# Kernel tuning notes

Measured on AMD Instinct MI355X. Metric: run time of the kernel, lower is better.

Reference implementation:

```python
import jax, jax.numpy as jnp
import numpy as np

C = 64
NUM_GROUPS = 16  # per Normalize() logic for in_channels=64
EPS = 1e-5

def group_norm(x, gamma, beta):
    b, c, h, w, d = x.shape
    xg = x.reshape(b, NUM_GROUPS, c // NUM_GROUPS, h, w, d)
    mean = xg.mean(axis=(2, 3, 4, 5), keepdims=True)
    var = xg.var(axis=(2, 3, 4, 5), keepdims=True)
    xg = (xg - mean) * jax.lax.rsqrt(var + EPS)
    xn = xg.reshape(b, c, h, w, d)
    return xn * gamma[None, :, None, None, None] + beta[None, :, None, None, None]

def conv1x1(x, w, b):
    # 1x1x1 conv3d == channel mixing: w is [out_c, in_c]
    return jnp.einsum('bchwd,oc->bohwd', x, w) + b[None, :, None, None, None]

def setup_inputs() -> dict:
    key = jax.random.key(0)
    ks = jax.random.split(key, 11)
    s = 1.0 / np.sqrt(C)
    return {
        'x': jax.random.normal(ks[0], (2, C, 16, 16, 16), dtype=jnp.float32),
        'norm_w': jnp.ones((C,), jnp.float32),
        'norm_b': jnp.zeros((C,), jnp.float32),
        'q_w': jax.random.uniform(ks[1], (C, C), jnp.float32, -s, s),
        'q_b': jax.random.uniform(ks[2], (C,), jnp.float32, -s, s),
        'k_w': jax.random.uniform(ks[3], (C, C), jnp.float32, -s, s),
        'k_b': jax.random.uniform(ks[4], (C,), jnp.float32, -s, s),
        'v_w': jax.random.uniform(ks[5], (C, C), jnp.float32, -s, s),
        'v_b': jax.random.uniform(ks[6], (C,), jnp.float32, -s, s),
        'proj_w': jax.random.uniform(ks[7], (C, C), jnp.float32, -s, s),
        'proj_b': jax.random.uniform(ks[8], (C,), jnp.float32, -s, s),
    }

def reference(x, norm_w, norm_b, q_w, q_b, k_w, k_b, v_w, v_b, proj_w, proj_b):
    b, c, h, w, d = x.shape
    n = h * w * d
    hn = group_norm(x, norm_w, norm_b)
    q = conv1x1(hn, q_w, q_b).reshape(b, c, n)   # [b, c, n]
    k = conv1x1(hn, k_w, k_b).reshape(b, c, n)
    v = conv1x1(hn, v_w, v_b).reshape(b, c, n)
    scale = c ** (-0.5)
    scores = jnp.einsum('bcq,bck->bqk', q, k) * scale   # [b, n_q, n_k]
    attn = jax.nn.softmax(scores, axis=2)
    out = jnp.einsum('bck,bqk->bcq', v, attn)            # [b, c, n]
    out = out.reshape(b, c, h, w, d)
    out = conv1x1(out, proj_w, proj_b)
    return x + out
```

## Files before the change

kernel.cpp:

```cpp
#include <hip/hip_runtime.h>
#include <hip/hip_bf16.h>

#define B 2
#define C 64
#define N 4096
#define EPS 1e-5f
#define QSCALE_LOG2E 0.18033688f

using short8 = __attribute__((ext_vector_type(8))) short;
using f32x16 = __attribute__((ext_vector_type(16))) float;

__device__ inline short f2bf(float f) {
  __hip_bfloat16 h = __float2bfloat16(f);
  union { __hip_bfloat16 h; short s; } u; u.h = h; return u.s;
}
__device__ inline float bf2f(short s) {
  union { unsigned u; float f; } u;
  u.u = ((unsigned)(unsigned short)s) << 16;
  return u.f;
}
__device__ inline int packbf(float a, float b) {
  return (int)((unsigned short)f2bf(a) | ((unsigned)(unsigned short)f2bf(b) << 16));
}

__global__ __launch_bounds__(256) void gn_part_kernel(
    const float* __restrict__ x, float2* __restrict__ part) {
  int blk = blockIdx.x;
  int bg = blk >> 4, sl = blk & 15;
  const float4* xv = (const float4*)(x + (size_t)bg * 4 * N) + sl * 256;
  int tid = threadIdx.x;
  float4 v = xv[tid];
  float s = v.x + v.y + v.z + v.w;
  float s2 = v.x * v.x + v.y * v.y + v.z * v.z + v.w * v.w;
  __shared__ float ss[256], ss2[256];
  ss[tid] = s; ss2[tid] = s2;
  __syncthreads();
  for (int st = 128; st > 0; st >>= 1) {
    if (tid < st) { ss[tid] += ss[tid + st]; ss2[tid] += ss2[tid + st]; }
    __syncthreads();
  }
  if (tid == 0) part[blk] = make_float2(ss[0], ss2[0]);
}

__global__ __launch_bounds__(128) void gn_final_kernel(
    const float2* __restrict__ part, const float* __restrict__ gw,
    const float* __restrict__ gb, float* __restrict__ ascale,
    float* __restrict__ bshift) {
  int t = threadIdx.x;
  int c = t & 63, b = t >> 6, g = c >> 2;
  int bg = b * 16 + g;
  float s = 0.f, s2 = 0.f;
#pragma unroll
  for (int sl = 0; sl < 16; ++sl) {
    float2 p = part[bg * 16 + sl];
    s += p.x; s2 += p.y;
  }
  float mean = s * (1.f / 16384.f);
  float var = s2 * (1.f / 16384.f) - mean * mean;
  float inv = rsqrtf(var + EPS);
  float a = inv * gw[c];
  ascale[t] = a;
  bshift[t] = gb[c] - mean * a;
}

__global__ __launch_bounds__(256) void qkv_kernel(
    const float* __restrict__ x, const float* __restrict__ ascale,
    const float* __restrict__ bshift,
    const float* __restrict__ qw, const float* __restrict__ qb,
    const float* __restrict__ kw, const float* __restrict__ kb,
    const float* __restrict__ vw, const float* __restrict__ vb,
    short* __restrict__ q_t, short* __restrict__ k_t, short* __restrict__ v_b) {
  int o0 = blockIdx.y * 8, b = blockIdx.z;
  int pos = blockIdx.x * 256 + threadIdx.x;
  const float* xp = x + (size_t)b * C * N + pos;
  const float* as = ascale + b * C;
  const float* bs = bshift + b * C;

  float sq[8], sk[8], sv[8];
#pragma unroll
  for (int j = 0; j < 8; ++j) { sq[j] = 0.f; sk[j] = 0.f; sv[j] = 0.f; }
#pragma unroll
  for (int c = 0; c < C; ++c) {
    float hv = fmaf(xp[(size_t)c * N], as[c], bs[c]);
#pragma unroll
    for (int j = 0; j < 8; ++j) {
      sq[j] = fmaf(qw[(o0 + j) * C + c], hv, sq[j]);
      sk[j] = fmaf(kw[(o0 + j) * C + c], hv, sk[j]);
      sv[j] = fmaf(vw[(o0 + j) * C + c], hv, sv[j]);
    }
  }
  size_t ti = ((size_t)b * N + pos) * C;
  short8 qv, kv;
#pragma unroll
  for (int j = 0; j < 8; ++j) {
    qv[j] = f2bf((sq[j] + qb[o0 + j]) * QSCALE_LOG2E);
    kv[j] = f2bf(sk[j] + kb[o0 + j]);
  }
  *(short8*)&q_t[ti + o0] = qv;
  *(short8*)&k_t[ti + o0] = kv;
#pragma unroll
  for (int j = 0; j < 8; ++j)
    v_b[((size_t)b * C + o0 + j) * N + pos] = f2bf(sv[j] + vb[o0 + j]);
}

__device__ inline void softpack(f32x16& s, int hi, float& lsum,
                                short8& p0, short8& p1) {
  float ps = 0.f;
#pragma unroll
  for (int i = 0; i < 16; ++i) { s[i] = exp2f(s[i]); ps += s[i]; }
  lsum += ps;
  union U { int i[4]; short8 v; } f0, f1;
  {
    int x0 = packbf(s[0], s[1]), z0 = packbf(s[2], s[3]);
    int y0 = packbf(s[4], s[5]), w0 = packbf(s[6], s[7]);
    int xs = __shfl_xor(x0, 32), zs = __shfl_xor(z0, 32);
    int ys = __shfl_xor(y0, 32), ws2 = __shfl_xor(w0, 32);
    f0.i[0] = hi ? ys : x0; f0.i[1] = hi ? ws2 : z0;
    f0.i[2] = hi ? y0 : xs; f0.i[3] = hi ? w0 : zs;
  }
  {
    int x0 = packbf(s[8], s[9]), z0 = packbf(s[10], s[11]);
    int y0 = packbf(s[12], s[13]), w0 = packbf(s[14], s[15]);
    int xs = __shfl_xor(x0, 32), zs = __shfl_xor(z0, 32);
    int ys = __shfl_xor(y0, 32), ws2 = __shfl_xor(w0, 32);
    f1.i[0] = hi ? ys : x0; f1.i[1] = hi ? ws2 : z0;
    f1.i[2] = hi ? y0 : xs; f1.i[3] = hi ? w0 : zs;
  }
  p0 = f0.v; p1 = f1.v;
}

__global__ __launch_bounds__(256) void attn_kernel(
    const short* __restrict__ q_t, const short* __restrict__ k_t,
    const short* __restrict__ v_b, short* __restrict__ opart,
    float* __restrict__ lpart, int segLen, int kseg) {
  int b = blockIdx.z, s = blockIdx.y;
  int l = threadIdx.x & 63;
  int q0 = blockIdx.x * 256 + (threadIdx.x >> 6) * 64;
  int lo5 = l & 31;
  int hi = l >> 5;

  const short* qp = q_t + (size_t)b * N * C;
  const short* kp = k_t + (size_t)b * N * C;
  const short* vp = v_b + (size_t)b * C * N;

  short8 qf[2][4];
#pragma unroll
  for (int qt = 0; qt < 2; ++qt)
#pragma unroll
    for (int t = 0; t < 4; ++t)
      qf[qt][t] = *(const short8*)&qp[(size_t)(q0 + qt * 32 + lo5) * C + t * 16 + hi * 8];

  f32x16 oacc00, oacc01, oacc10, oacc11;
#pragma unroll
  for (int i = 0; i < 16; ++i) { oacc00[i] = 0.f; oacc01[i] = 0.f; oacc10[i] = 0.f; oacc11[i] = 0.f; }
  float lsum[2] = {0.f, 0.f};

  int kbase = s * segLen;

#define LOAD_KF(DST, K0)                                                     \
  _Pragma("unroll") for (int t = 0; t < 4; ++t)                              \
      DST[t] = *(const short8*)&kp[(size_t)((K0) + lo5) * C + t * 16 + hi * 8];
#define LOAD_VF(DST, K0)                                                     \
  DST[0] = *(const short8*)&vp[(size_t)(lo5) * N + (K0) + hi * 8];           \
  DST[1] = *(const short8*)&vp[(size_t)(32 + lo5) * N + (K0) + hi * 8];      \
  DST[2] = *(const short8*)&vp[(size_t)(lo5) * N + (K0) + 16 + hi * 8];      \
  DST[3] = *(const short8*)&vp[(size_t)(32 + lo5) * N + (K0) + 16 + hi * 8];

#define CHUNK(KF, VF)                                                        \
  {                                                                          \
    f32x16 s0_, s1_;                                                         \
    _Pragma("unroll") for (int i = 0; i < 16; ++i) { s0_[i] = 0.f; s1_[i] = 0.f; } \
    __builtin_amdgcn_s_setprio(1);                                           \
    _Pragma("unroll") for (int t = 0; t < 4; ++t) {                          \
      s0_ = __builtin_amdgcn_mfma_f32_32x32x16_bf16(KF[t], qf[0][t], s0_, 0, 0, 0); \
      s1_ = __builtin_amdgcn_mfma_f32_32x32x16_bf16(KF[t], qf[1][t], s1_, 0, 0, 0); \
    }                                                                        \
    __builtin_amdgcn_s_setprio(0);                                           \
    short8 pf00, pf01, pf10, pf11;                                           \
    softpack(s0_, hi, lsum[0], pf00, pf01);                                  \
    softpack(s1_, hi, lsum[1], pf10, pf11);                                  \
    __builtin_amdgcn_s_setprio(1);                                           \
    oacc00 = __builtin_amdgcn_mfma_f32_32x32x16_bf16(VF[0], pf00, oacc00, 0, 0, 0); \
    oacc01 = __builtin_amdgcn_mfma_f32_32x32x16_bf16(VF[1], pf00, oacc01, 0, 0, 0); \
    oacc10 = __builtin_amdgcn_mfma_f32_32x32x16_bf16(VF[0], pf10, oacc10, 0, 0, 0); \
    oacc11 = __builtin_amdgcn_mfma_f32_32x32x16_bf16(VF[1], pf10, oacc11, 0, 0, 0); \
    oacc00 = __builtin_amdgcn_mfma_f32_32x32x16_bf16(VF[2], pf01, oacc00, 0, 0, 0); \
    oacc01 = __builtin_amdgcn_mfma_f32_32x32x16_bf16(VF[3], pf01, oacc01, 0, 0, 0); \
    oacc10 = __builtin_amdgcn_mfma_f32_32x32x16_bf16(VF[2], pf11, oacc10, 0, 0, 0); \
    oacc11 = __builtin_amdgcn_mfma_f32_32x32x16_bf16(VF[3], pf11, oacc11, 0, 0, 0); \
    __builtin_amdgcn_s_setprio(0);                                           \
  }

  short8 kf0[4], kf1[4], vf0[4], vf1[4];
  LOAD_KF(kf0, kbase)
  LOAD_VF(vf0, kbase)

  for (int kc = 0; kc < segLen; kc += 64) {
    int kA = kbase + kc;
    LOAD_KF(kf1, kA + 32)
    LOAD_VF(vf1, kA + 32)
    CHUNK(kf0, vf0)
    int kN = (kc + 64 < segLen) ? (kA + 64) : kA;
    LOAD_KF(kf0, kN)
    LOAD_VF(vf0, kN)
    CHUNK(kf1, vf1)
  }

#pragma unroll
  for (int qt = 0; qt < 2; ++qt) {
    lsum[qt] += __shfl_xor(lsum[qt], 32);
    int qq = q0 + qt * 32 + lo5;
    short* op = opart + (size_t)(b * kseg + s) * C * N;
#pragma unroll
    for (int r = 0; r < 16; ++r) {
      int c = (r & 3) + 8 * (r >> 2) + 4 * hi;
      float v0 = (qt == 0) ? oacc00[r] : oacc10[r];
      float v1 = (qt == 0) ? oacc01[r] : oacc11[r];
      op[(size_t)c * N + qq] = f2bf(v0);
      op[(size_t)(c + 32) * N + qq] = f2bf(v1);
    }
    if (hi == 0) lpart[(size_t)(b * kseg + s) * N + qq] = lsum[qt];
  }
#undef LOAD_KF
#undef LOAD_VF
#undef CHUNK
}

__global__ __launch_bounds__(256) void merge_kernel(
    const short* __restrict__ opart, const float* __restrict__ lpart,
    short* __restrict__ attnout, int kseg) {
  int idx = blockIdx.x * 256 + threadIdx.x;
  int q4 = (idx & 1023) * 4;
  int c = (idx >> 10) & 63;
  int b = idx >> 16;

  float o[4] = {0.f, 0.f, 0.f, 0.f};
  float L[4] = {0.f, 0.f, 0.f, 0.f};
  for (int s = 0; s < kseg; ++s) {
    float4 lv = *(const float4*)&lpart[(size_t)(b * kseg + s) * N + q4];
    L[0] += lv.x; L[1] += lv.y; L[2] += lv.z; L[3] += lv.w;
    short4 ov = *(const short4*)&opart[((size_t)(b * kseg + s) * C + c) * N + q4];
    o[0] += bf2f(ov.x); o[1] += bf2f(ov.y); o[2] += bf2f(ov.z); o[3] += bf2f(ov.w);
  }
  short4 r;
  r.x = f2bf(o[0] / L[0]); r.y = f2bf(o[1] / L[1]);
  r.z = f2bf(o[2] / L[2]); r.w = f2bf(o[3] / L[3]);
  *(short4*)&attnout[(size_t)(b * C + c) * N + q4] = r;
}

__global__ __launch_bounds__(256) void proj_kernel(
    const short* __restrict__ at, const float* __restrict__ pw,
    const float* __restrict__ pb, const float* __restrict__ x,
    float* __restrict__ out) {
  int o0 = blockIdx.y * 8, b = blockIdx.z;
  int pos = blockIdx.x * 256 + threadIdx.x;
  const short* h = at + (size_t)b * C * N + pos;
  float sum[8];
#pragma unroll
  for (int j = 0; j < 8; ++j) sum[j] = 0.f;
#pragma unroll
  for (int c = 0; c < C; ++c) {
    float hv = bf2f(h[(size_t)c * N]);
#pragma unroll
    for (int j = 0; j < 8; ++j) sum[j] = fmaf(pw[(o0 + j) * C + c], hv, sum[j]);
  }
#pragma unroll
  for (int j = 0; j < 8; ++j) {
    size_t oi = (size_t)(b * C + o0 + j) * N + pos;
    out[oi] = x[oi] + sum[j] + pb[o0 + j];
  }
}

extern "C" void kernel_launch(void* const* d_in, const int* in_sizes, int n_in,
                              void* d_out, int out_size, void* d_ws, size_t ws_size,
                              hipStream_t stream) {
  const float* x      = (const float*)d_in[0];
  const float* norm_w = (const float*)d_in[1];
  const float* norm_b = (const float*)d_in[2];
  const float* q_w    = (const float*)d_in[3];
  const float* q_b    = (const float*)d_in[4];
  const float* k_w    = (const float*)d_in[5];
  const float* k_b    = (const float*)d_in[6];
  const float* v_w    = (const float*)d_in[7];
  const float* v_b    = (const float*)d_in[8];
  const float* proj_w = (const float*)d_in[9];
  const float* proj_b = (const float*)d_in[10];
  float* out = (float*)d_out;

  const size_t BCN = (size_t)B * C * N;

  int kseg = 16;
  auto need = [&](int s) -> size_t {
    return BCN * 2 * 4
         + (2 * B * C + 1024 + (size_t)s * B * N) * 4
         + (size_t)s * BCN * 2;
  };
  while (kseg > 1 && need(kseg) > ws_size) kseg >>= 1;
  int segLen = N / kseg;

  short* q_t     = (short*)d_ws;
  short* k_t     = q_t + BCN;
  short* vbuf    = k_t + BCN;
  short* attnout = vbuf + BCN;
  float* ascale  = (float*)(attnout + BCN);
  float* bshift  = ascale + B * C;
  float2* part   = (float2*)(bshift + B * C);
  float* lpart   = (float*)(part + 512);
  short* opart   = (short*)(lpart + (size_t)kseg * B * N);

  gn_part_kernel<<<512, 256, 0, stream>>>(x, part);
  gn_final_kernel<<<1, 128, 0, stream>>>(part, norm_w, norm_b, ascale, bshift);

  qkv_kernel<<<dim3(N / 256, C / 8, B), 256, 0, stream>>>(
      x, ascale, bshift, q_w, q_b, k_w, k_b, v_w, v_b, q_t, k_t, vbuf);

  attn_kernel<<<dim3(N / 256, kseg, B), 256, 0, stream>>>(
      q_t, k_t, vbuf, opart, lpart, segLen, kseg);

  merge_kernel<<<(int)(BCN / 4 / 256), 256, 0, stream>>>(
      opart, lpart, attnout, kseg);

  proj_kernel<<<dim3(N / 256, C / 8, B), 256, 0, stream>>>(
      attnout, proj_w, proj_b, x, out);
}
```

Measured before the change: 77.09 us.

## Fuse GN finalize into QKV, merge into projection, and simplify attention loop

New measurement: 92.95 us. 1.21x slower.

```diff
diff --git a/kernel.cpp b/kernel.cpp
--- a/kernel.cpp
+++ b/kernel.cpp
@@ -5,6 +5,8 @@
 #define C 64
 #define N 4096
 #define EPS 1e-5f
+#define KSEG 16
+#define SEGLEN 256
 #define QSCALE_LOG2E 0.18033688f
 
 using short8 = __attribute__((ext_vector_type(8))) short;
@@ -19,8 +21,10 @@
   u.u = ((unsigned)(unsigned short)s) << 16;
   return u.f;
 }
-__device__ inline int packbf(float a, float b) {
-  return (int)((unsigned short)f2bf(a) | ((unsigned)(unsigned short)f2bf(b) << 16));
+__device__ inline int cvtpk(float a, float b) {
+  int r;
+  asm("v_cvt_pk_bf16_f32 %0, %1, %2" : "=v"(r) : "v"(a), "v"(b));
+  return r;
 }
 
 __global__ __launch_bounds__(256) void gn_part_kernel(
@@ -42,46 +46,44 @@
   if (tid == 0) part[blk] = make_float2(ss[0], ss2[0]);
 }
 
-__global__ __launch_bounds__(128) void gn_final_kernel(
-    const float2* __restrict__ part, const float* __restrict__ gw,
-    const float* __restrict__ gb, float* __restrict__ ascale,
-    float* __restrict__ bshift) {
-  int t = threadIdx.x;
-  int c = t & 63, b = t >> 6, g = c >> 2;
-  int bg = b * 16 + g;
-  float s = 0.f, s2 = 0.f;
-#pragma unroll
-  for (int sl = 0; sl < 16; ++sl) {
-    float2 p = part[bg * 16 + sl];
-    s += p.x; s2 += p.y;
-  }
-  float mean = s * (1.f / 16384.f);
-  float var = s2 * (1.f / 16384.f) - mean * mean;
-  float inv = rsqrtf(var + EPS);
-  float a = inv * gw[c];
-  ascale[t] = a;
-  bshift[t] = gb[c] - mean * a;
-}
-
 __global__ __launch_bounds__(256) void qkv_kernel(
-    const float* __restrict__ x, const float* __restrict__ ascale,
-    const float* __restrict__ bshift,
+    const float* __restrict__ x, const float2* __restrict__ part,
+    const float* __restrict__ gw, const float* __restrict__ gb,
     const float* __restrict__ qw, const float* __restrict__ qb,
     const float* __restrict__ kw, const float* __restrict__ kb,
     const float* __restrict__ vw, const float* __restrict__ vb,
     short* __restrict__ q_t, short* __restrict__ k_t, short* __restrict__ v_b) {
   int o0 = blockIdx.y * 8, b = blockIdx.z;
-  int pos = blockIdx.x * 256 + threadIdx.x;
+  int tid = threadIdx.x;
+
+  __shared__ float asl[C], bsl[C];
+  if (tid < C) {
+    int c = tid, g = c >> 2;
+    int bg = b * 16 + g;
+    float s = 0.f, s2 = 0.f;
+#pragma unroll
+    for (int sl = 0; sl < 16; ++sl) {
+      float2 p = part[bg * 16 + sl];
+      s += p.x; s2 += p.y;
+    }
+    float mean = s * (1.f / 16384.f);
+    float var = s2 * (1.f / 16384.f) - mean * mean;
+    float inv = rsqrtf(var + EPS);
+    float a = inv * gw[c];
+    asl[c] = a;
+    bsl[c] = gb[c] - mean * a;
+  }
+  __syncthreads();
+
+  int pos = blockIdx.x * 256 + tid;
   const float* xp = x + (size_t)b * C * N + pos;
-  const float* as = ascale + b * C;
-  const float* bs = bshift + b * C;
 
   float sq[8], sk[8], sv[8];
 #pragma unroll
   for (int j = 0; j < 8; ++j) { sq[j] = 0.f; sk[j] = 0.f; sv[j] = 0.f; }
 #pragma unroll
   for (int c = 0; c < C; ++c) {
-    float hv = fmaf(xp[(size_t)c * N], as[c], bs[c]);
+    float hv = fmaf(xp[(size_t)c * N], asl[c], bsl[c]);
 #pragma unroll
     for (int j = 0; j < 8; ++j) {
       sq[j] = fmaf(qw[(o0 + j) * C + c], hv, sq[j]);
@@ -111,16 +113,16 @@
   lsum += ps;
   union U { int i[4]; short8 v; } f0, f1;
   {
-    int x0 = packbf(s[0], s[1]), z0 = packbf(s[2], s[3]);
-    int y0 = packbf(s[4], s[5]), w0 = packbf(s[6], s[7]);
+    int x0 = cvtpk(s[0], s[1]), z0 = cvtpk(s[2], s[3]);
+    int y0 = cvtpk(s[4], s[5]), w0 = cvtpk(s[6], s[7]);
     int xs = __shfl_xor(x0, 32), zs = __shfl_xor(z0, 32);
     int ys = __shfl_xor(y0, 32), ws2 = __shfl_xor(w0, 32);
     f0.i[0] = hi ? ys : x0; f0.i[1] = hi ? ws2 : z0;
     f0.i[2] = hi ? y0 : xs; f0.i[3] = hi ? w0 : zs;
   }
   {
-    int x0 = packbf(s[8], s[9]), z0 = packbf(s[10], s[11]);
-    int y0 = packbf(s[12], s[13]), w0 = packbf(s[14], s[15]);
+    int x0 = cvtpk(s[8], s[9]), z0 = cvtpk(s[10], s[11]);
+    int y0 = cvtpk(s[12], s[13]), w0 = cvtpk(s[14], s[15]);
     int xs = __shfl_xor(x0, 32), zs = __shfl_xor(z0, 32);
     int ys = __shfl_xor(y0, 32), ws2 = __shfl_xor(w0, 32);
     f1.i[0] = hi ? ys : x0; f1.i[1] = hi ? ws2 : z0;
@@ -129,10 +131,10 @@
   p0 = f0.v; p1 = f1.v;
 }
 
-__global__ __launch_bounds__(256) void attn_kernel(
+__global__ __launch_bounds__(256, 2) void attn_kernel(
     const short* __restrict__ q_t, const short* __restrict__ k_t,
     const short* __restrict__ v_b, short* __restrict__ opart,
-    float* __restrict__ lpart, int segLen, int kseg) {
+    float* __restrict__ lpart) {
   int b = blockIdx.z, s = blockIdx.y;
   int l = threadIdx.x & 63;
   int q0 = blockIdx.x * 256 + (threadIdx.x >> 6) * 64;
@@ -155,62 +157,51 @@
   for (int i = 0; i < 16; ++i) { oacc00[i] = 0.f; oacc01[i] = 0.f; oacc10[i] = 0.f; oacc11[i] = 0.f; }
   float lsum[2] = {0.f, 0.f};
 
-  int kbase = s * segLen;
-
-#define LOAD_KF(DST, K0)                                                     \
-  _Pragma("unroll") for (int t = 0; t < 4; ++t)                              \
-      DST[t] = *(const short8*)&kp[(size_t)((K0) + lo5) * C + t * 16 + hi * 8];
-#define LOAD_VF(DST, K0)                                                     \
-  DST[0] = *(const short8*)&vp[(size_t)(lo5) * N + (K0) + hi * 8];           \
-  DST[1] = *(const short8*)&vp[(size_t)(32 + lo5) * N + (K0) + hi * 8];      \
-  DST[2] = *(const short8*)&vp[(size_t)(lo5) * N + (K0) + 16 + hi * 8];      \
-  DST[3] = *(const short8*)&vp[(size_t)(32 + lo5) * N + (K0) + 16 + hi * 8];
-
-#define CHUNK(KF, VF)                                                        \
-  {                                                                          \
-    f32x16 s0_, s1_;                                                         \
-    _Pragma("unroll") for (int i = 0; i < 16; ++i) { s0_[i] = 0.f; s1_[i] = 0.f; } \
-    __builtin_amdgcn_s_setprio(1);                                           \
-    _Pragma("unroll") for (int t = 0; t < 4; ++t) {                          \
-      s0_ = __builtin_amdgcn_mfma_f32_32x32x16_bf16(KF[t], qf[0][t], s0_, 0, 0, 0); \
-      s1_ = __builtin_amdgcn_mfma_f32_32x32x16_bf16(KF[t], qf[1][t], s1_, 0, 0, 0); \
-    }                                                                        \
-    __builtin_amdgcn_s_setprio(0);                                           \
-    short8 pf00, pf01, pf10, pf11;                                           \
-    softpack(s0_, hi, lsum[0], pf00, pf01);                                  \
-    softpack(s1_, hi, lsum[1], pf10, pf11);                                  \
-    __builtin_amdgcn_s_setprio(1);                                           \
-    oacc00 = __builtin_amdgcn_mfma_f32_32x32x16_bf16(VF[0], pf00, oacc00, 0, 0, 0); \
-    oacc01 = __builtin_amdgcn_mfma_f32_32x32x16_bf16(VF[1], pf00, oacc01, 0, 0, 0); \
-    oacc10 = __builtin_amdgcn_mfma_f32_32x32x16_bf16(VF[0], pf10, oacc10, 0, 0, 0); \
-    oacc11 = __builtin_amdgcn_mfma_f32_32x32x16_bf16(VF[1], pf10, oacc11, 0, 0, 0); \
-    oacc00 = __builtin_amdgcn_mfma_f32_32x32x16_bf16(VF[2], pf01, oacc00, 0, 0, 0); \
-    oacc01 = __builtin_amdgcn_mfma_f32_32x32x16_bf16(VF[3], pf01, oacc01, 0, 0, 0); \
-    oacc10 = __builtin_amdgcn_mfma_f32_32x32x16_bf16(VF[2], pf11, oacc10, 0, 0, 0); \
-    oacc11 = __builtin_amdgcn_mfma_f32_32x32x16_bf16(VF[3], pf11, oacc11, 0, 0, 0); \
-    __builtin_amdgcn_s_setprio(0);                                           \
-  }
-
-  short8 kf0[4], kf1[4], vf0[4], vf1[4];
-  LOAD_KF(kf0, kbase)
-  LOAD_VF(vf0, kbase)
-
-  for (int kc = 0; kc < segLen; kc += 64) {
-    int kA = kbase + kc;
-    LOAD_KF(kf1, kA + 32)
-    LOAD_VF(vf1, kA + 32)
-    CHUNK(kf0, vf0)
-    int kN = (kc + 64 < segLen) ? (kA + 64) : kA;
-    LOAD_KF(kf0, kN)
-    LOAD_VF(vf0, kN)
-    CHUNK(kf1, vf1)
+  int kbase = s * SEGLEN;
+  for (int kc = 0; kc < SEGLEN; kc += 32) {
+    int k0 = kbase + kc;
+    short8 kf[4];
+#pragma unroll
+    for (int t = 0; t < 4; ++t)
+      kf[t] = *(const short8*)&kp[(size_t)(k0 + lo5) * C + t * 16 + hi * 8];
+    short8 vf[4];
+    vf[0] = *(const short8*)&vp[(size_t)(lo5) * N + k0 + hi * 8];
+    vf[1] = *(const short8*)&vp[(size_t)(32 + lo5) * N + k0 + hi * 8];
+    vf[2] = *(const short8*)&vp[(size_t)(lo5) * N + k0 + 16 + hi * 8];
+    vf[3] = *(const short8*)&vp[(size_t)(32 + lo5) * N + k0 + 16 + hi * 8];
+
+    f32x16 sacc[2];
+#pragma unroll
+    for (int i = 0; i < 16; ++i) { sacc[0][i] = 0.f; sacc[1][i] = 0.f; }
+    __builtin_amdgcn_s_setprio(1);
+#pragma unroll
+    for (int t = 0; t < 4; ++t) {
+      sacc[0] = __builtin_amdgcn_mfma_f32_32x32x16_bf16(kf[t], qf[0][t], sacc[0], 0, 0, 0);
+      sacc[1] = __builtin_amdgcn_mfma_f32_32x32x16_bf16(kf[t], qf[1][t], sacc[1], 0, 0, 0);
+    }
+    __builtin_amdgcn_s_setprio(0);
+
+    short8 pf00, pf01, pf10, pf11;
+    softpack(sacc[0], hi, lsum[0], pf00, pf01);
+    softpack(sacc[1], hi, lsum[1], pf10, pf11);
+
+    __builtin_amdgcn_s_setprio(1);
+    oacc00 = __builtin_amdgcn_mfma_f32_32x32x16_bf16(vf[0], pf00, oacc00, 0, 0, 0);
+    oacc01 = __builtin_amdgcn_mfma_f32_32x32x16_bf16(vf[1], pf00, oacc01, 0, 0, 0);
+    oacc10 = __builtin_amdgcn_mfma_f32_32x32x16_bf16(vf[0], pf10, oacc10, 0, 0, 0);
+    oacc11 = __builtin_amdgcn_mfma_f32_32x32x16_bf16(vf[1], pf10, oacc11, 0, 0, 0);
+    oacc00 = __builtin_amdgcn_mfma_f32_32x32x16_bf16(vf[2], pf01, oacc00, 0, 0, 0);
+    oacc01 = __builtin_amdgcn_mfma_f32_32x32x16_bf16(vf[3], pf01, oacc01, 0, 0, 0);
+    oacc10 = __builtin_amdgcn_mfma_f32_32x32x16_bf16(vf[2], pf11, oacc10, 0, 0, 0);
+    oacc11 = __builtin_amdgcn_mfma_f32_32x32x16_bf16(vf[3], pf11, oacc11, 0, 0, 0);
+    __builtin_amdgcn_s_setprio(0);
   }
 
 #pragma unroll
   for (int qt = 0; qt < 2; ++qt) {
     lsum[qt] += __shfl_xor(lsum[qt], 32);
     int qq = q0 + qt * 32 + lo5;
-    short* op = opart + (size_t)(b * kseg + s) * C * N;
+    short* op = opart + (size_t)(b * KSEG + s) * C * N;
 #pragma unroll
     for (int r = 0; r < 16; ++r) {
       int c = (r & 3) + 8 * (r >> 2) + 4 * hi;
@@ -219,55 +210,43 @@
       op[(size_t)c * N + qq] = f2bf(v0);
       op[(size_t)(c + 32) * N + qq] = f2bf(v1);
     }
-    if (hi == 0) lpart[(size_t)(b * kseg + s) * N + qq] = lsum[qt];
-  }
-#undef LOAD_KF
-#undef LOAD_VF
-#undef CHUNK
-}
-
-__global__ __launch_bounds__(256) void merge_kernel(
+    if (hi == 0) lpart[(size_t)(b * KSEG + s) * N + qq] = lsum[qt];
+  }
+}
+
+__global__ __launch_bounds__(256) void mergeproj_kernel(
     const short* __restrict__ opart, const float* __restrict__ lpart,
-    short* __restrict__ attnout, int kseg) {
-  int idx = blockIdx.x * 256 + threadIdx.x;
-  int q4 = (idx & 1023) * 4;
-  int c = (idx >> 10) & 63;
-  int b = idx >> 16;
-
-  float o[4] = {0.f, 0.f, 0.f, 0.f};
-  float L[4] = {0.f, 0.f, 0.f, 0.f};
-  for (int s = 0; s < kseg; ++s) {
-    float4 lv = *(const float4*)&lpart[(size_t)(b * kseg + s) * N + q4];
-    L[0] += lv.x; L[1] += lv.y; L[2] += lv.z; L[3] += lv.w;
-    short4 ov = *(const short4*)&opart[((size_t)(b * kseg + s) * C + c) * N + q4];
-    o[0] += bf2f(ov.x); o[1] += bf2f(ov.y); o[2] += bf2f(ov.z); o[3] += bf2f(ov.w);
-  }
-  short4 r;
-  r.x = f2bf(o[0] / L[0]); r.y = f2bf(o[1] / L[1]);
-  r.z = f2bf(o[2] / L[2]); r.w = f2bf(o[3] / L[3]);
-  *(short4*)&attnout[(size_t)(b * C + c) * N + q4] = r;
-}
-
-__global__ __launch_bounds__(256) void proj_kernel(
-    const short* __restrict__ at, const float* __restrict__ pw,
-    const float* __restrict__ pb, const float* __restrict__ x,
-    float* __restrict__ out) {
-  int o0 = blockIdx.y * 8, b = blockIdx.z;
-  int pos = blockIdx.x * 256 + threadIdx.x;
-  const short* h = at + (size_t)b * C * N + pos;
-  float sum[8];
-#pragma unroll
-  for (int j = 0; j < 8; ++j) sum[j] = 0.f;
+    const float* __restrict__ pw, const float* __restrict__ pb,
+    const float* __restrict__ x, float* __restrict__ out) {
+  int b = blockIdx.z;
+  int pos = blockIdx.x * 64 + (threadIdx.x & 63);
+  int o0 = blockIdx.y * 32 + (threadIdx.x >> 6) * 8;
+
+  float L = 0.f;
+#pragma unroll
+  for (int s = 0; s < KSEG; ++s) L += lpart[(size_t)(b * KSEG + s) * N + pos];
+  float invL = 1.f / L;
+
+  float acc[8];
+#pragma unroll
+  for (int j = 0; j < 8; ++j) acc[j] = 0.f;
+
+  const short* opb = opart + (size_t)b * KSEG * C * N + pos;
 #pragma unroll
   for (int c = 0; c < C; ++c) {
-    float hv = bf2f(h[(size_t)c * N]);
-#pragma unroll
-    for (int j = 0; j < 8; ++j) sum[j] = fmaf(pw[(o0 + j) * C + c], hv, sum[j]);
+    float a = 0.f;
+#pragma unroll
+    for (int s = 0; s < KSEG; ++s)
+      a += bf2f(opb[((size_t)s * C + c) * N]);
+    a *= invL;
+#pragma unroll
+    for (int j = 0; j < 8; ++j)
+      acc[j] = fmaf(pw[(o0 + j) * C + c], a, acc[j]);
   }
 #pragma unroll
   for (int j = 0; j < 8; ++j) {
     size_t oi = (size_t)(b * C + o0 + j) * N + pos;
-    out[oi] = x[oi] + sum[j] + pb[o0 + j];
+    out[oi] = x[oi] + acc[j] + pb[o0 + j];
   }
 }
 
@@ -288,38 +267,21 @@
   float* out = (float*)d_out;
 
   const size_t BCN = (size_t)B * C * N;
-
-  int kseg = 16;
-  auto need = [&](int s) -> size_t {
-    return BCN * 2 * 4
-         + (2 * B * C + 1024 + (size_t)s * B * N) * 4
-         + (size_t)s * BCN * 2;
-  };
-  while (kseg > 1 && need(kseg) > ws_size) kseg >>= 1;
-  int segLen = N / kseg;
-
-  short* q_t     = (short*)d_ws;
-  short* k_t     = q_t + BCN;
-  short* vbuf    = k_t + BCN;
-  short* attnout = vbuf + BCN;
-  float* ascale  = (float*)(attnout + BCN);
-  float* bshift  = ascale + B * C;
-  float2* part   = (float2*)(bshift + B * C);
-  float* lpart   = (float*)(part + 512);
-  short* opart   = (short*)(lpart + (size_t)kseg * B * N);
+  short* q_t   = (short*)d_ws;
+  short* k_t   = q_t + BCN;
+  short* vbuf  = k_t + BCN;
+  float2* part = (float2*)(vbuf + BCN);
+  float* lpart = (float*)(part + 512);
+  short* opart = (short*)(lpart + (size_t)KSEG * B * N);
 
   gn_part_kernel<<<512, 256, 0, stream>>>(x, part);
-  gn_final_kernel<<<1, 128, 0, stream>>>(part, norm_w, norm_b, ascale, bshift);
 
   qkv_kernel<<<dim3(N / 256, C / 8, B), 256, 0, stream>>>(
-      x, ascale, bshift, q_w, q_b, k_w, k_b, v_w, v_b, q_t, k_t, vbuf);
-
-  attn_kernel<<<dim3(N / 256, kseg, B), 256, 0, stream>>>(
-      q_t, k_t, vbuf, opart, lpart, segLen, kseg);
-
-  merge_kernel<<<(int)(BCN / 4 / 256), 256, 0, stream>>>(
-      opart, lpart, attnout, kseg);
-
-  proj_kernel<<<dim3(N / 256, C / 8, B), 256, 0, stream>>>(
-      attnout, proj_w, proj_b, x, out);
-}
+      x, part, norm_w, norm_b, q_w, q_b, k_w, k_b, v_w, v_b, q_t, k_t, vbuf);
+
+  attn_kernel<<<dim3(N / 256, KSEG, B), 256, 0, stream>>>(
+      q_t, k_t, vbuf, opart, lpart);
+
+  mergeproj_kernel<<<dim3(N / 64, 2, B), 256, 0, stream>>>(
+      opart, lpart, proj_w, proj_b, x, out);
+}
```
